# Kernel optimization log

Hardware: AMD Instinct MI355X
Metric: run time of the kernel (lower is better)

The kernel has to match this reference:

```python
import jax, jax.numpy as jnp
import numpy as np

B, S, D = 4, 4096, 256

def setup_inputs() -> dict:
    key = jax.random.key(0)
    k1, k2, k3, k4 = jax.random.split(key, 4)
    inputs = jax.random.normal(k1, (B, S, D), dtype=jnp.float32)
    Wq = jax.random.normal(k2, (D, D), dtype=jnp.float32) * 0.05
    Wk = jax.random.normal(k3, (D, D), dtype=jnp.float32) * 0.05
    Wv = jax.random.normal(k4, (D, D), dtype=jnp.float32) * 0.05
    return {"inputs": inputs, "Wq": Wq, "Wk": Wk, "Wv": Wv}

def reference(inputs, Wq, Wk, Wv):
    # single-head self-attention: softmax(QK^T / sqrt(d)) V
    d = inputs.shape[-1]
    Q = jnp.einsum('bsd,de->bse', inputs, Wq)
    K = jnp.einsum('bsd,de->bse', inputs, Wk)
    V = jnp.einsum('bsd,de->bse', inputs, Wv)
    scale = 1.0 / jnp.sqrt(jnp.asarray(d, dtype=inputs.dtype))
    scores = jnp.einsum('bqe,bke->bqk', Q, K) * scale  # [B,S,S]
    attn = jax.nn.softmax(scores, axis=-1)
    return jnp.einsum('bqk,bke->bqe', attn, V)
```

## Files before the change

kernel.cpp:

```cpp
#include <hip/hip_runtime.h>
#include <hip/hip_bf16.h>

typedef __attribute__((ext_vector_type(8))) short bfrag_t;
typedef __attribute__((ext_vector_type(4))) short s4_t;
typedef __attribute__((ext_vector_type(4))) float facc_t;
typedef __attribute__((ext_vector_type(16))) float f16acc_t;
typedef __attribute__((ext_vector_type(4))) int i4_t;

#define B_ 4
#define S_ 4096
#define D_ 256

using gas_v = const __attribute__((address_space(1))) void;
using las_v = __attribute__((address_space(3))) void;

__device__ __forceinline__ short f2bf(float f) {
  union { float fv; unsigned u; } x; x.fv = f;
  unsigned r = x.u + 0x7FFFu + ((x.u >> 16) & 1u);
  return (short)(r >> 16);
}

__device__ __forceinline__ int cvtpk(float lo, float hi) {
  int r;
  asm("v_cvt_pk_bf16_f32 %0, %1, %2" : "=v"(r) : "v"(lo), "v"(hi));
  return r;
}

__device__ __forceinline__ facc_t mfma16(bfrag_t a, bfrag_t b, facc_t c) {
  return __builtin_amdgcn_mfma_f32_16x16x32_bf16(a, b, c, 0, 0, 0);
}
__device__ __forceinline__ f16acc_t mfma32(bfrag_t a, bfrag_t b, f16acc_t c) {
  return __builtin_amdgcn_mfma_f32_32x32x16_bf16(a, b, c, 0, 0, 0);
}

__global__ void wt_kernel(const float* __restrict__ Wq, const float* __restrict__ Wk,
                          const float* __restrict__ Wv, short* __restrict__ WT) {
  const int p = blockIdx.x >> 4;
  const float* W = (p == 0) ? Wq : ((p == 1) ? Wk : Wv);
  short* o = WT + p * (D_ * D_);
  const int e = (blockIdx.x & 15) * 16 + (threadIdx.x >> 4);
  const int td = threadIdx.x & 15;
  #pragma unroll
  for (int dd = 0; dd < 16; ++dd) {
    int d = td * 16 + dd;
    o[e * D_ + d] = f2bf(W[d * D_ + e]);
  }
}

__global__ __launch_bounds__(256) void proj_kernel(
    const float* __restrict__ X, const short* __restrict__ WT,
    short* __restrict__ Qb, short* __restrict__ Kb, short* __restrict__ VT) {
  __shared__ __align__(16) short Stg[256 * 72];
  const int tid  = threadIdx.x;
  const int wave = tid >> 6, lane = tid & 63;
  const int lrow = lane & 15, kch = lane >> 4;
  const int p  = blockIdx.x >> 8;
  const int rb = blockIdx.x & 255;
  const int row0 = rb * 64 + wave * 16;
  const int arow = row0 + lrow;
  const int bblk = rb >> 6;

  bfrag_t af[8];
  #pragma unroll
  for (int kt = 0; kt < 8; ++kt) {
    const float* src = X + (size_t)arow * D_ + kt * 32 + kch * 8;
    float4 a = *reinterpret_cast<const float4*>(src);
    float4 b = *reinterpret_cast<const float4*>(src + 4);
    bfrag_t f;
    f[0] = f2bf(a.x); f[1] = f2bf(a.y); f[2] = f2bf(a.z); f[3] = f2bf(a.w);
    f[4] = f2bf(b.x); f[5] = f2bf(b.y); f[6] = f2bf(b.z); f[7] = f2bf(b.w);
    af[kt] = f;
  }

  const short* Wp = WT + p * (D_ * D_);
  facc_t acc[16];
  #pragma unroll
  for (int nt = 0; nt < 16; ++nt) acc[nt] = (facc_t)0.0f;
  #pragma unroll
  for (int kt = 0; kt < 8; ++kt) {
    #pragma unroll
    for (int nt = 0; nt < 16; ++nt) {
      bfrag_t bf = *reinterpret_cast<const bfrag_t*>(
          Wp + (nt * 16 + lrow) * D_ + kt * 32 + kch * 8);
      acc[nt] = mfma16(af[kt], bf, acc[nt]);
    }
  }
  if (p < 2) {
    const float sc = (p == 0) ? 0.0625f : 1.0f;
    #pragma unroll
    for (int nt = 0; nt < 16; ++nt)
      #pragma unroll
      for (int r = 0; r < 4; ++r)
        Stg[(wave * 16 + kch * 4 + r) * 264 + nt * 16 + lrow] =
            f2bf(acc[nt][r] * sc);
    __syncthreads();
    short* dstbase = ((p == 0) ? Qb : Kb) + (size_t)rb * 64 * D_;
    #pragma unroll
    for (int k = 0; k < 8; ++k) {
      int c = k * 256 + tid;
      int row = c >> 5, col = c & 31;
      *reinterpret_cast<bfrag_t*>(dstbase + row * D_ + col * 8) =
          *reinterpret_cast<const bfrag_t*>(&Stg[row * 264 + col * 8]);
    }
  } else {
    #pragma unroll
    for (int nt = 0; nt < 16; ++nt) {
      s4_t v;
      #pragma unroll
      for (int r = 0; r < 4; ++r) v[r] = f2bf(acc[nt][r]);
      *reinterpret_cast<s4_t*>(
          &Stg[(nt * 16 + lrow) * 72 + (wave >> 1) * 32 + (wave & 1) * 16 +
               (kch & 1) * 8 + (kch >> 1) * 4]) = v;
    }
    __syncthreads();
    const int d = tid;
    const int s0 = (rb & 63) * 64;
    short* dst = VT + ((size_t)(bblk * D_ + d)) * S_ + s0;
    #pragma unroll
    for (int j = 0; j < 8; ++j)
      *reinterpret_cast<bfrag_t*>(dst + j * 8) =
          *reinterpret_cast<const bfrag_t*>(&Stg[d * 72 + j * 8]);
  }
}

template<int SPLIT>
__global__ __launch_bounds__(256, 2) void attn32(
    const short* __restrict__ Qb, const short* __restrict__ Kb,
    const short* __restrict__ VT, float* __restrict__ P0,
    float* __restrict__ PX, float2* __restrict__ ML) {
  __shared__ __align__(16) short Kl[2][32 * 256];
  __shared__ __align__(16) short Vl[2][256 * 32];
  const int tid  = threadIdx.x;
  const int wave = tid >> 6, lane = tid & 63;
  const int l31 = lane & 31, hi = lane >> 5;
  const int ksw = (lane & 7) << 4;
  const int vsw = ((l31 >> 1) & 3) << 4;
  const int hw = blockIdx.x;
  const int g = hw & 7, rest = hw >> 3;
  int b, part, qblk;
  if constexpr (SPLIT == 4)      { b = g >> 1; part = (g & 1) * 2 + (rest & 1); qblk = rest >> 1; }
  else if constexpr (SPLIT == 2) { b = g >> 1; part = g & 1;                    qblk = rest; }
  else                           { b = g >> 1; part = 0;                qblk = (g & 1) * 16 + rest; }
  const int q0 = qblk * 128 + wave * 32;
  const int kvbase = part * (S_ / SPLIT);
  constexpr int STEPS = (S_ / SPLIT) / 32;

  const short* Kbp = Kb + (size_t)b * S_ * D_ + (size_t)kvbase * D_;
  const short* Vbp = VT + (size_t)b * D_ * S_ + kvbase;

  bfrag_t qf[16];
  const short* Qp = Qb + ((size_t)b * S_ + q0 + l31) * D_;
  #pragma unroll
  for (int kt = 0; kt < 16; ++kt)
    qf[kt] = *reinterpret_cast<const bfrag_t*>(Qp + kt * 16 + hi * 8);

  auto stage = [&](int bf, int kv0) {
    #pragma unroll
    for (int j = 0; j < 4; ++j) {
      int L = j * 4096 + tid * 16;
      int row = L >> 9;
      int cs = (L & 511) ^ ((row & 7) << 4);
      const short* src = Kbp + (size_t)(kv0 + row) * D_ + (cs >> 1);
      short* dst = &Kl[bf][(j * 4096 + wave * 1024) >> 1];
      __builtin_amdgcn_global_load_lds((gas_v*)src, (las_v*)dst, 16, 0, 0);
    }
    #pragma unroll
    for (int j = 0; j < 4; ++j) {
      int L = j * 4096 + tid * 16;
      int d = L >> 6;
      int cs = (L & 63) ^ (((d >> 1) & 3) << 4);
      const short* src = Vbp + (size_t)d * S_ + kv0 + (cs >> 1);
      short* dst = &Vl[bf][(j * 4096 + wave * 1024) >> 1];
      __builtin_amdgcn_global_load_lds((gas_v*)src, (las_v*)dst, 16, 0, 0);
    }
  };

  f16acc_t o32[8];
  #pragma unroll
  for (int nt = 0; nt < 8; ++nt) o32[nt] = (f16acc_t)0.0f;
  float mrow = -3.0e38f, lsum = 0.0f;

  stage(0, 0);
  asm volatile("s_waitcnt vmcnt(0)" ::: "memory");
  __syncthreads();
  int buf = 0;

  #pragma unroll 1
  for (int t = 0; t < STEPS; ++t) {
    if (t < STEPS - 1) stage(buf ^ 1, (t + 1) * 32);
    f16acc_t s16 = (f16acc_t)0.0f;
    const char* Kbase = (const char*)&Kl[buf][0];
    __builtin_amdgcn_s_setprio(1);
    #pragma unroll
    for (int kt = 0; kt < 16; ++kt) {
      bfrag_t kf = *reinterpret_cast<const bfrag_t*>(
          Kbase + l31 * 512 + ((kt * 32 + hi * 16) ^ ksw));
      s16 = mfma32(kf, qf[kt], s16);
    }
    __builtin_amdgcn_s_setprio(0);
    float mx = s16[0];
    #pragma unroll
    for (int i = 1; i < 16; ++i) mx = fmaxf(mx, s16[i]);
    mx = fmaxf(mx, __shfl_xor(mx, 32));
    if (mx > mrow + 8.0f) {
      float sf = __expf(mrow - mx);
      mrow = mx;
      lsum *= sf;
      #pragma unroll
      for (int nt = 0; nt < 8; ++nt) o32[nt] *= sf;
    }
    float pe[16];
    float ls = 0.0f;
    #pragma unroll
    for (int i = 0; i < 16; ++i) {
      pe[i] = __expf(s16[i] - mrow);
      ls += pe[i];
    }
    lsum += ls;
    i4_t w0, w1;
    w0.x = cvtpk(pe[0], pe[1]);  w0.y = cvtpk(pe[2], pe[3]);
    w0.z = cvtpk(pe[4], pe[5]);  w0.w = cvtpk(pe[6], pe[7]);
    w1.x = cvtpk(pe[8], pe[9]);  w1.y = cvtpk(pe[10], pe[11]);
    w1.z = cvtpk(pe[12], pe[13]); w1.w = cvtpk(pe[14], pe[15]);
    bfrag_t pb0 = __builtin_bit_cast(bfrag_t, w0);
    bfrag_t pb1 = __builtin_bit_cast(bfrag_t, w1);
    const char* Vbase = (const char*)&Vl[buf][0];
    __builtin_amdgcn_s_setprio(1);
    #pragma unroll
    for (int nt = 0; nt < 8; ++nt) {
      const char* vb = Vbase + (nt * 32 + l31) * 64;
      bfrag_t v0 = *reinterpret_cast<const bfrag_t*>(vb + ((hi * 16) ^ vsw));
      o32[nt] = mfma32(v0, pb0, o32[nt]);
      bfrag_t v1 = *reinterpret_cast<const bfrag_t*>(vb + ((32 + hi * 16) ^ vsw));
      o32[nt] = mfma32(v1, pb1, o32[nt]);
    }
    __builtin_amdgcn_s_setprio(0);
    asm volatile("s_waitcnt vmcnt(0)" ::: "memory");
    __syncthreads();
    buf ^= 1;
  }

  lsum += __shfl_xor(lsum, 32);
  float* Pd = (SPLIT == 1 || part == 0)
                  ? P0 : PX + (size_t)(part - 1) * ((size_t)B_ * S_ * D_);
  float* Og = Pd + ((size_t)b * S_ + q0 + l31) * D_;
  if constexpr (SPLIT == 1) {
    float inv = 1.0f / lsum;
    #pragma unroll
    for (int nt = 0; nt < 8; ++nt)
      #pragma unroll
      for (int gg = 0; gg < 4; ++gg) {
        float4 o;
        o.x = o32[nt][gg * 4 + 0] * inv; o.y = o32[nt][gg * 4 + 1] * inv;
        o.z = o32[nt][gg * 4 + 2] * inv; o.w = o32[nt][gg * 4 + 3] * inv;
        *reinterpret_cast<float4*>(Og + nt * 32 + hi * 4 + gg * 8) = o;
      }
  } else {
    #pragma unroll
    for (int nt = 0; nt < 8; ++nt)
      #pragma unroll
      for (int gg = 0; gg < 4; ++gg) {
        float4 o;
        o.x = o32[nt][gg * 4 + 0]; o.y = o32[nt][gg * 4 + 1];
        o.z = o32[nt][gg * 4 + 2]; o.w = o32[nt][gg * 4 + 3];
        *reinterpret_cast<float4*>(Og + nt * 32 + hi * 4 + gg * 8) = o;
      }
    if (lane < 32) {
      float2 ml; ml.x = mrow; ml.y = lsum;
      ML[part * (B_ * S_) + b * S_ + q0 + l31] = ml;
    }
  }
}

template<int SPLIT>
__global__ __launch_bounds__(256) void combineN(
    const float* __restrict__ PX, const float2* __restrict__ ML,
    float* __restrict__ Out) {
  const int r = blockIdx.x * 4 + (threadIdx.x >> 6);
  const int d4 = (threadIdx.x & 63) * 4;
  float2 ml[SPLIT];
  #pragma unroll
  for (int p = 0; p < SPLIT; ++p) ml[p] = ML[p * (B_ * S_) + r];
  float m = ml[0].x;
  #pragma unroll
  for (int p = 1; p < SPLIT; ++p) m = fmaxf(m, ml[p].x);
  float w[SPLIT];
  float denom = 0.0f;
  #pragma unroll
  for (int p = 0; p < SPLIT; ++p) {
    w[p] = __expf(ml[p].x - m);
    denom += ml[p].y * w[p];
  }
  float inv = 1.0f / denom;
  size_t idx = (size_t)r * D_ + d4;
  float4 x = *reinterpret_cast<float4*>(Out + idx);
  float4 acc;
  acc.x = x.x * w[0]; acc.y = x.y * w[0]; acc.z = x.z * w[0]; acc.w = x.w * w[0];
  #pragma unroll
  for (int p = 1; p < SPLIT; ++p) {
    float4 y = *reinterpret_cast<const float4*>(
        PX + (size_t)(p - 1) * ((size_t)B_ * S_ * D_) + idx);
    acc.x += y.x * w[p]; acc.y += y.y * w[p];
    acc.z += y.z * w[p]; acc.w += y.w * w[p];
  }
  acc.x *= inv; acc.y *= inv; acc.z *= inv; acc.w *= inv;
  *reinterpret_cast<float4*>(Out + idx) = acc;
}

extern "C" void kernel_launch(void* const* d_in, const int* in_sizes, int n_in,
                              void* d_out, int out_size, void* d_ws, size_t ws_size,
                              hipStream_t stream) {
  const float* X  = (const float*)d_in[0];
  const float* Wq = (const float*)d_in[1];
  const float* Wk = (const float*)d_in[2];
  const float* Wv = (const float*)d_in[3];
  float* out = (float*)d_out;

  char* ws = (char*)d_ws;
  short* Qb = (short*)(ws);
  short* Kb = (short*)(ws + 8388608);
  short* VT = (short*)(ws + 16777216);
  short* WT = (short*)(ws + 25165824);
  float2* ML = (float2*)(ws + 25690112);
  float* PX  = (float*)(ws + 26214400);
  const size_t NP = (size_t)B_ * S_ * D_ * 4;
  const size_t need4 = 26214400 + 3 * NP;
  const size_t need2 = 26214400 + 1 * NP;

  wt_kernel<<<48, 256, 0, stream>>>(Wq, Wk, Wv, WT);
  proj_kernel<<<768, 256, 0, stream>>>(X, WT, Qb, Kb, VT);
  if (ws_size >= need4) {
    attn32<4><<<512, 256, 0, stream>>>(Qb, Kb, VT, out, PX, ML);
    combineN<4><<<(B_ * S_) / 4, 256, 0, stream>>>(PX, ML, out);
  } else if (ws_size >= need2) {
    attn32<2><<<256, 256, 0, stream>>>(Qb, Kb, VT, out, PX, ML);
    combineN<2><<<(B_ * S_) / 4, 256, 0, stream>>>(PX, ML, out);
  } else {
    attn32<1><<<128, 256, 0, stream>>>(Qb, Kb, VT, out, PX, (float2*)out);
  }
}
```

Measured before the change: 158.2 us.

## Fold log2e into Q scale, use raw exp2, transpose weights via LDS

The Q projection scale now includes log2(e), so the softmax can call the hardware v_exp_f32 (base-2) directly instead of __expf, which saves a multiply per element. The lazy-rescale threshold is raised to match the base-2 domain, and the row max uses a tree reduction. The weight transpose kernel now stages a tile in LDS to get coalesced reads and vectorized writes, though it launches fewer blocks. The combine kernel uses the same base-2 exponent, which stays consistent because the stored maxima are in log2 units.

Result: no change. 158.2 us (-0.0%).

```diff
diff --git a/kernel.cpp b/kernel.cpp
--- a/kernel.cpp
+++ b/kernel.cpp
@@ -26,6 +26,12 @@
   return r;
 }
 
+__device__ __forceinline__ float fexp2(float x) {
+  float r;
+  asm("v_exp_f32 %0, %1" : "=v"(r) : "v"(x));
+  return r;
+}
+
 __device__ __forceinline__ facc_t mfma16(bfrag_t a, bfrag_t b, facc_t c) {
   return __builtin_amdgcn_mfma_f32_16x16x32_bf16(a, b, c, 0, 0, 0);
 }
@@ -33,17 +39,32 @@
   return __builtin_amdgcn_mfma_f32_32x32x16_bf16(a, b, c, 0, 0, 0);
 }
 
-__global__ void wt_kernel(const float* __restrict__ Wq, const float* __restrict__ Wk,
-                          const float* __restrict__ Wv, short* __restrict__ WT) {
-  const int p = blockIdx.x >> 4;
+__global__ __launch_bounds__(256) void wt_kernel(
+    const float* __restrict__ Wq, const float* __restrict__ Wk,
+    const float* __restrict__ Wv, short* __restrict__ WT) {
+  __shared__ short Tl[256 * 68];
+  const int p = blockIdx.x >> 2;
+  const int estripe = (blockIdx.x & 3) * 64;
   const float* W = (p == 0) ? Wq : ((p == 1) ? Wk : Wv);
   short* o = WT + p * (D_ * D_);
-  const int e = (blockIdx.x & 15) * 16 + (threadIdx.x >> 4);
-  const int td = threadIdx.x & 15;
-  #pragma unroll
-  for (int dd = 0; dd < 16; ++dd) {
-    int d = td * 16 + dd;
-    o[e * D_ + d] = f2bf(W[d * D_ + e]);
+  const int el = threadIdx.x & 63, dq = threadIdx.x >> 6;
+  #pragma unroll 16
+  for (int pass = 0; pass < 64; ++pass) {
+    int d = pass * 4 + dq;
+    Tl[d * 68 + el] = f2bf(W[d * 256 + estripe + el]);
+  }
+  __syncthreads();
+  const int eo = threadIdx.x >> 2, qd = threadIdx.x & 3;
+  #pragma unroll
+  for (int j = 0; j < 8; ++j) {
+    s4_t a, b2;
+    #pragma unroll
+    for (int t2 = 0; t2 < 4; ++t2) a[t2]  = Tl[(qd * 64 + j * 8 + t2) * 68 + eo];
+    #pragma unroll
+    for (int t2 = 0; t2 < 4; ++t2) b2[t2] = Tl[(qd * 64 + j * 8 + 4 + t2) * 68 + eo];
+    short* dst = o + (estripe + eo) * 256 + qd * 64 + j * 8;
+    *reinterpret_cast<s4_t*>(dst) = a;
+    *reinterpret_cast<s4_t*>(dst + 4) = b2;
   }
 }
 
@@ -86,7 +107,7 @@
     }
   }
   if (p < 2) {
-    const float sc = (p == 0) ? 0.0625f : 1.0f;
+    const float sc = (p == 0) ? 0.09016844f : 1.0f;
     #pragma unroll
     for (int nt = 0; nt < 16; ++nt)
       #pragma unroll
@@ -198,12 +219,17 @@
       s16 = mfma32(kf, qf[kt], s16);
     }
     __builtin_amdgcn_s_setprio(0);
-    float mx = s16[0];
-    #pragma unroll
-    for (int i = 1; i < 16; ++i) mx = fmaxf(mx, s16[i]);
+    float a0 = fmaxf(fmaxf(s16[0], s16[1]), s16[2]);
+    float a1 = fmaxf(fmaxf(s16[3], s16[4]), s16[5]);
+    float a2 = fmaxf(fmaxf(s16[6], s16[7]), s16[8]);
+    float a3 = fmaxf(fmaxf(s16[9], s16[10]), s16[11]);
+    float a4 = fmaxf(fmaxf(s16[12], s16[13]), s16[14]);
+    float b0 = fmaxf(fmaxf(a0, a1), a2);
+    float b1 = fmaxf(fmaxf(a3, a4), s16[15]);
+    float mx = fmaxf(b0, b1);
     mx = fmaxf(mx, __shfl_xor(mx, 32));
-    if (mx > mrow + 8.0f) {
-      float sf = __expf(mrow - mx);
+    if (mx > mrow + 11.0f) {
+      float sf = fexp2(mrow - mx);
       mrow = mx;
       lsum *= sf;
       #pragma unroll
@@ -213,7 +239,7 @@
     float ls = 0.0f;
     #pragma unroll
     for (int i = 0; i < 16; ++i) {
-      pe[i] = __expf(s16[i] - mrow);
+      pe[i] = fexp2(s16[i] - mrow);
       ls += pe[i];
     }
     lsum += ls;
@@ -288,7 +314,7 @@
   float denom = 0.0f;
   #pragma unroll
   for (int p = 0; p < SPLIT; ++p) {
-    w[p] = __expf(ml[p].x - m);
+    w[p] = fexp2(ml[p].x - m);
     denom += ml[p].y * w[p];
   }
   float inv = 1.0f / denom;
@@ -327,7 +353,7 @@
   const size_t need4 = 26214400 + 3 * NP;
   const size_t need2 = 26214400 + 1 * NP;
 
-  wt_kernel<<<48, 256, 0, stream>>>(Wq, Wk, Wv, WT);
+  wt_kernel<<<12, 256, 0, stream>>>(Wq, Wk, Wv, WT);
   proj_kernel<<<768, 256, 0, stream>>>(X, WT, Qb, Kb, VT);
   if (ws_size >= need4) {
     attn32<4><<<512, 256, 0, stream>>>(Qb, Kb, VT, out, PX, ML);
```
